# Optimization experiments

Hardware: AMD Instinct MI355X
Metric: run time of the kernel (lower is better)

Reference implementation:

```python
import jax, jax.numpy as jnp
import numpy as np

MODEL_DIM = 1024
NUM_HEADS = 16
DEPTH = MODEL_DIM // NUM_HEADS


def setup_inputs() -> dict:
    key = jax.random.key(0)
    ks = jax.random.split(key, 9)
    B, S, D = 4, 2048, MODEL_DIM
    scale = 1.0 / np.sqrt(D)
    x = jax.random.normal(ks[0], (B, S, D), dtype=jnp.float32)
    wq = jax.random.normal(ks[1], (D, D), dtype=jnp.float32) * scale
    bq = jnp.zeros((D,), dtype=jnp.float32)
    wk = jax.random.normal(ks[2], (D, D), dtype=jnp.float32) * scale
    bk = jnp.zeros((D,), dtype=jnp.float32)
    wv = jax.random.normal(ks[3], (D, D), dtype=jnp.float32) * scale
    bv = jnp.zeros((D,), dtype=jnp.float32)
    wo = jax.random.normal(ks[4], (D, D), dtype=jnp.float32) * scale
    bo = jnp.zeros((D,), dtype=jnp.float32)
    return {"x": x, "wq": wq, "bq": bq, "wk": wk, "bk": bk,
            "wv": wv, "bv": bv, "wo": wo, "bo": bo}


def reference(x, wq, bq, wk, bk, wv, bv, wo, bo):
    B, S, D = x.shape
    H, dh = NUM_HEADS, DEPTH
    # projections
    q = (x @ wq + bq).reshape(B, S, H, dh).transpose(0, 2, 1, 3)  # [B,H,S,dh]
    k = (x @ wk + bk).reshape(B, S, H, dh).transpose(0, 2, 1, 3)
    v = (x @ wv + bv).reshape(B, S, H, dh).transpose(0, 2, 1, 3)
    # scaled dot-product attention (full score matrix, as in source)
    logits = jnp.einsum('bhqd,bhkd->bhqk', q, k) / jnp.sqrt(jnp.float32(dh))
    attn = jax.nn.softmax(logits, axis=-1)
    out = jnp.einsum('bhqk,bhkd->bhqd', attn, v)  # [B,H,S,dh]
    out = out.transpose(0, 2, 1, 3).reshape(B, S, D)
    return out @ wo + bo
```

## Files before the change

kernel.cpp:

```cpp
#include <hip/hip_runtime.h>
#include <hip/hip_bf16.h>


#define S_LEN 2048
#define DMODEL 1024
#define NH 16
#define DH 64
#define BATCH 4
#define MROWS (BATCH * S_LEN)
#define NELEM_X (MROWS * DMODEL)
#define NELEM_W (DMODEL * DMODEL)
#define NELEM_B DMODEL

typedef short short8 __attribute__((ext_vector_type(8)));
typedef float floatx4 __attribute__((ext_vector_type(4)));
typedef float floatx16 __attribute__((ext_vector_type(16)));

__device__ __forceinline__ float bf2f(unsigned short u) {
    union { unsigned int i; float f; } c; c.i = ((unsigned int)u) << 16; return c.f;
}
__device__ __forceinline__ unsigned int f2bf_pk(float lo, float hi) {
    unsigned int r;
    asm("v_cvt_pk_bf16_f32 %0, %1, %2" : "=v"(r) : "v"(lo), "v"(hi));
    return r;
}
__device__ __forceinline__ void async_copy16(const void* g, void* l) {
    __builtin_amdgcn_global_load_lds(
        (const __attribute__((address_space(1))) unsigned int*)g,
        (__attribute__((address_space(3))) unsigned int*)l, 16, 0, 0);
}

__device__ __forceinline__ floatx16 mfma32_k16(short8 a, short8 b, floatx16 c) {
    return __builtin_amdgcn_mfma_f32_32x32x16_bf16(a, b, c, 0, 0, 0);
}

__global__ void sniff_kernel(const unsigned short* __restrict__ x, int* flag) {
    __shared__ int cnt;
    if (threadIdx.x == 0) cnt = 0;
    __syncthreads();
    int c = 0;
    for (int i = threadIdx.x; i < 65536; i += 256) {
        unsigned int e = (x[i] >> 7) & 0xFFu;
        if (e >= 0xC0u) c++;
    }
    atomicAdd(&cnt, c);
    __syncthreads();
    if (threadIdx.x == 0) *flag = (cnt > 64) ? 1 : 0;
}

struct ConvArgs { const void* s[5]; unsigned short* d[5]; int n8[5]; };
__global__ void convert_all(ConvArgs a, const int* __restrict__ flag) {
    const int seg = blockIdx.y;
    const int f = *flag;
    const int n8 = a.n8[seg];
    unsigned short* dst = a.d[seg];
    int i = blockIdx.x * blockDim.x + threadIdx.x;
    const int stride = gridDim.x * blockDim.x;
    if (f) {
        const float4* s4 = (const float4*)a.s[seg];
        for (; i < n8; i += stride) {
            float4 x0 = s4[2 * i], x1 = s4[2 * i + 1];
            uint4 o;
            o.x = f2bf_pk(x0.x, x0.y); o.y = f2bf_pk(x0.z, x0.w);
            o.z = f2bf_pk(x1.x, x1.y); o.w = f2bf_pk(x1.z, x1.w);
            *(uint4*)(dst + (size_t)i * 8) = o;
        }
    } else {
        const uint4* s4 = (const uint4*)a.s[seg];
        for (; i < n8; i += stride) *(uint4*)(dst + (size_t)i * 8) = s4[i];
    }
}

struct TWArgs { const void* s[4]; unsigned short* d[4]; };
__global__ void transpose_w(TWArgs a, const int* __restrict__ flag) {
    __shared__ unsigned int Lt[64 * 33];
    const int z = blockIdx.z;
    const int f = *flag;
    const int k0 = blockIdx.x * 64, n0 = blockIdx.y * 64;
    const int t = threadIdx.x;
    const int c = t & 63, rgrp = t >> 6;

    if (f) {
        const float* W = (const float*)a.s[z];
        #pragma unroll
        for (int s = 0; s < 8; s++) {
            int r0 = rgrp * 16 + 2 * s;
            float v0 = W[(size_t)(k0 + r0) * DMODEL + n0 + c];
            float v1 = W[(size_t)(k0 + r0 + 1) * DMODEL + n0 + c];
            Lt[c * 33 + rgrp * 8 + s] = f2bf_pk(v0, v1);
        }
    } else {
        const unsigned short* W = (const unsigned short*)a.s[z];
        #pragma unroll
        for (int s = 0; s < 8; s++) {
            int r0 = rgrp * 16 + 2 * s;
            unsigned int lo = W[(size_t)(k0 + r0) * DMODEL + n0 + c];
            unsigned int hi = W[(size_t)(k0 + r0 + 1) * DMODEL + n0 + c];
            Lt[c * 33 + rgrp * 8 + s] = lo | (hi << 16);
        }
    }
    __syncthreads();
    const int row = t >> 2, j = t & 3;
    unsigned int* outp = (unsigned int*)(a.d[z] + (size_t)(n0 + row) * DMODEL + k0);
    #pragma unroll
    for (int i = 0; i < 8; i++) outp[j * 8 + i] = Lt[row * 33 + j * 8 + i];
}

__global__ void transpose_v(const unsigned short* __restrict__ vws,
                            unsigned short* __restrict__ vt) {
    __shared__ unsigned int Lt[64 * 33];
    const int tok0 = blockIdx.x * 64;
    const int bh   = blockIdx.y;
    const int b    = bh >> 4;
    const int h    = bh & 15;
    const int t = threadIdx.x;
    const int c = t & 63, rgrp = t >> 6;

    const unsigned short* src = vws + (size_t)b * S_LEN * DMODEL + h * DH;
    #pragma unroll
    for (int s = 0; s < 8; s++) {
        int r0 = rgrp * 16 + 2 * s;
        unsigned int lo = src[(size_t)(tok0 + r0) * DMODEL + c];
        unsigned int hi = src[(size_t)(tok0 + r0 + 1) * DMODEL + c];
        Lt[c * 33 + rgrp * 8 + s] = lo | (hi << 16);
    }
    __syncthreads();
    const int row = t >> 2, j = t & 3;
    unsigned int* outp = (unsigned int*)(vt + (size_t)bh * DH * S_LEN
                                            + (size_t)row * S_LEN + tok0);
    const int p2[8] = {0, 1, 4, 5, 2, 3, 6, 7};
    #pragma unroll
    for (int i = 0; i < 8; i++) outp[j * 8 + i] = Lt[row * 33 + j * 8 + p2[i]];
}

__global__ __launch_bounds__(256, 2)
void gemm_bias_kernel(const unsigned short* __restrict__ X,
                      const unsigned short* __restrict__ T0, const unsigned short* __restrict__ B0, void* __restrict__ Y0,
                      const unsigned short* __restrict__ T1, const unsigned short* __restrict__ B1, void* __restrict__ Y1,
                      const unsigned short* __restrict__ T2, const unsigned short* __restrict__ B2, void* __restrict__ Y2,
                      float os0, float os1, float os2,
                      const int* __restrict__ flag, int fp32_out)
{
    const unsigned short* Wt = T0; const unsigned short* Bi = B0; void* Y = Y0;
    float os = os0;
    if (blockIdx.z == 1) { Wt = T1; Bi = B1; Y = Y1; os = os1; }
    else if (blockIdx.z == 2) { Wt = T2; Bi = B2; Y = Y2; os = os2; }
    const int f32o = fp32_out ? (*flag) : 0;

    __shared__ __align__(16) unsigned short As[128 * 32];
    __shared__ __align__(16) unsigned short Bs[128 * 32];

    const int t    = threadIdx.x;
    const int lane = t & 63;
    const int wid  = t >> 6;
    const int quad = lane >> 4;
    const int n16  = lane & 15;
    const int wm   = wid >> 1, wn = wid & 1;

    const int m0 = blockIdx.x * 128;
    const int n0 = blockIdx.y * 128;

    floatx4 acc[4][4];
    #pragma unroll
    for (int i = 0; i < 4; i++)
        #pragma unroll
        for (int j = 0; j < 4; j++) acc[i][j] = (floatx4){0.f, 0.f, 0.f, 0.f};

    const int r = t >> 2, c8 = (t & 3) * 8;

    for (int kb = 0; kb < DMODEL; kb += 32) {
        __syncthreads();
        async_copy16(X  + (size_t)(m0 + r)      * DMODEL + kb + c8, As + r * 32 + c8);
        async_copy16(X  + (size_t)(m0 + 64 + r) * DMODEL + kb + c8, As + (64 + r) * 32 + c8);
        async_copy16(Wt + (size_t)(n0 + r)      * DMODEL + kb + c8, Bs + r * 32 + c8);
        async_copy16(Wt + (size_t)(n0 + 64 + r) * DMODEL + kb + c8, Bs + (64 + r) * 32 + c8);
        __syncthreads();

        short8 af[4], bfr[4];
        #pragma unroll
        for (int mt = 0; mt < 4; mt++)
            af[mt] = *(const short8*)(As + (wm * 64 + mt * 16 + n16) * 32 + quad * 8);
        #pragma unroll
        for (int nt = 0; nt < 4; nt++)
            bfr[nt] = *(const short8*)(Bs + (wn * 64 + nt * 16 + n16) * 32 + quad * 8);
        #pragma unroll
        for (int mt = 0; mt < 4; mt++)
            #pragma unroll
            for (int nt = 0; nt < 4; nt++)
                acc[mt][nt] = __builtin_amdgcn_mfma_f32_16x16x32_bf16(af[mt], bfr[nt], acc[mt][nt], 0, 0, 0);
    }

    float bv4[4];
    #pragma unroll
    for (int nt = 0; nt < 4; nt++) bv4[nt] = bf2f(Bi[n0 + wn * 64 + nt * 16 + n16]) * os;
    #pragma unroll
    for (int mt = 0; mt < 4; mt++)
        #pragma unroll
        for (int rr = 0; rr < 4; rr++) {
            size_t row = (size_t)(m0 + wm * 64 + mt * 16 + quad * 4 + rr);
            if (f32o) {
                #pragma unroll
                for (int nt = 0; nt < 4; nt++) {
                    int col = n0 + wn * 64 + nt * 16 + n16;
                    ((float*)Y)[row * DMODEL + col] = fmaf(acc[mt][nt][rr], os, bv4[nt]);
                }
            } else {
                #pragma unroll
                for (int np = 0; np < 2; np++) {
                    float v0 = fmaf(acc[mt][2 * np    ][rr], os, bv4[2 * np]);
                    float v1 = fmaf(acc[mt][2 * np + 1][rr], os, bv4[2 * np + 1]);
                    unsigned int pk = f2bf_pk(v0, v1);
                    int col = n0 + wn * 64 + (2 * np) * 16 + n16;
                    ((unsigned short*)Y)[row * DMODEL + col]      = (unsigned short)pk;
                    ((unsigned short*)Y)[row * DMODEL + col + 16] = (unsigned short)(pk >> 16);
                }
            }
        }
}

__global__ __launch_bounds__(256, 2)
void attn_kernel(const unsigned short* Qw,
                 const unsigned short* __restrict__ Kw,
                 const unsigned short* __restrict__ VT,
                 unsigned short* Ow)
{
    __shared__ __align__(16) unsigned short Ks[64 * 64];
    __shared__ __align__(16) unsigned short Vts[64 * 64];

    const int t    = threadIdx.x;
    const int lane = t & 63;
    const int w    = t >> 6;
    const int q32  = lane & 31;
    const int hi   = lane >> 5;
    const int r7   = q32 & 7;

    const int bid  = blockIdx.x;
    const int bh   = bid & 63;
    const int qblk = bid >> 6;
    const int b    = bh >> 4;
    const int h    = bh & 15;

    const size_t baseRow = (size_t)b * S_LEN;
    const int hoff = h * DH;
    const unsigned short* VTb = VT + (size_t)bh * DH * S_LEN;

    int qrow[2];
    short8 qf[2][4];
    #pragma unroll
    for (int g = 0; g < 2; g++) {
        qrow[g] = qblk * 256 + w * 64 + g * 32 + q32;
        #pragma unroll
        for (int ds = 0; ds < 4; ds++)
            qf[g][ds] = *(const short8*)(Qw + (baseRow + qrow[g]) * DMODEL + hoff
                                            + ds * 16 + hi * 8);
    }

    const floatx16 z16 = {0.f,0.f,0.f,0.f,0.f,0.f,0.f,0.f,
                          0.f,0.f,0.f,0.f,0.f,0.f,0.f,0.f};
    const short8 ones8 = {(short)0x3F80, (short)0x3F80, (short)0x3F80, (short)0x3F80,
                          (short)0x3F80, (short)0x3F80, (short)0x3F80, (short)0x3F80};
    floatx16 acco[2][2];
    #pragma unroll
    for (int g = 0; g < 2; g++)
        #pragma unroll
        for (int dt = 0; dt < 2; dt++) acco[g][dt] = z16;
    floatx16 accl[2];
    accl[0] = z16; accl[1] = z16;

    const int srow = t >> 2;
    const int scc  = (t & 3) * 2;
    const int kswz0 = ((scc    ) ^ (srow & 7)) * 8;
    const int kswz1 = ((scc + 1) ^ (srow & 7)) * 8;
    unsigned short* KsW = Ks  + srow * 64;
    unsigned short* VsW = Vts + srow * 64;
    const unsigned short* Kp = Kw + (baseRow + srow) * DMODEL + hoff + scc * 8;
    const unsigned short* Vp = VTb + (size_t)srow * S_LEN + scc * 8;

    float4 kr0 = *(const float4*)(Kp);
    float4 kr1 = *(const float4*)(Kp + 8);
    float4 vr0 = *(const float4*)(Vp);
    float4 vr1 = *(const float4*)(Vp + 8);
    const unsigned short* KpL = Kp + (size_t)64 * DMODEL;
    const unsigned short* VpL = Vp + 64;

    for (int kb = 0; kb < S_LEN; kb += 64) {
        __syncthreads();
        *(float4*)(KsW + kswz0) = kr0;
        *(float4*)(KsW + kswz1) = kr1;
        *(float4*)(VsW + kswz0) = vr0;
        *(float4*)(VsW + kswz1) = vr1;
        if (kb + 64 < S_LEN) {
            kr0 = *(const float4*)(KpL);
            kr1 = *(const float4*)(KpL + 8);
            vr0 = *(const float4*)(VpL);
            vr1 = *(const float4*)(VpL + 8);
            KpL += (size_t)64 * DMODEL;
            VpL += 64;
        }
        __syncthreads();

        #pragma unroll
        for (int kt = 0; kt < 2; kt++) {
            const unsigned short* Kr = Ks + (kt * 32 + q32) * 64;
            floatx16 s0, s1;
            __builtin_amdgcn_s_setprio(1);
            {
                short8 kf = *(const short8*)(Kr + ((hi ^ r7) * 8));
                s0 = mfma32_k16(kf, qf[0][0], z16);
                s1 = mfma32_k16(kf, qf[1][0], z16);
            }
            #pragma unroll
            for (int ds = 1; ds < 4; ds++) {
                short8 kf = *(const short8*)(Kr + (((ds * 2 + hi) ^ r7) * 8));
                s0 = mfma32_k16(kf, qf[0][ds], s0);
                s1 = mfma32_k16(kf, qf[1][ds], s1);
            }
            __builtin_amdgcn_s_setprio(0);

            #pragma unroll
            for (int i = 0; i < 16; i++) {
                s0[i] = __builtin_exp2f(s0[i]);
                s1[i] = __builtin_exp2f(s1[i]);
            }

            __builtin_amdgcn_s_setprio(1);
            #pragma unroll
            for (int tt = 0; tt < 2; tt++) {
                union { unsigned int u[4]; short8 s8; } pb0, pb1;
                #pragma unroll
                for (int j = 0; j < 4; j++) {
                    pb0.u[j] = f2bf_pk(s0[8 * tt + 2 * j], s0[8 * tt + 2 * j + 1]);
                    pb1.u[j] = f2bf_pk(s1[8 * tt + 2 * j], s1[8 * tt + 2 * j + 1]);
                }
                const int vchunk = ((4 * kt + 2 * tt + hi) ^ r7) * 8;
                #pragma unroll
                for (int dt = 0; dt < 2; dt++) {
                    short8 vf = *(const short8*)(Vts + (dt * 32 + q32) * 64 + vchunk);
                    acco[0][dt] = mfma32_k16(vf, pb0.s8, acco[0][dt]);
                    acco[1][dt] = mfma32_k16(vf, pb1.s8, acco[1][dt]);
                }
                accl[0] = mfma32_k16(ones8, pb0.s8, accl[0]);
                accl[1] = mfma32_k16(ones8, pb1.s8, accl[1]);
            }
            __builtin_amdgcn_s_setprio(0);
        }
    }

    #pragma unroll
    for (int g = 0; g < 2; g++) {
        const float rinv = 1.f / accl[g][0];
        #pragma unroll
        for (int dt = 0; dt < 2; dt++) {
            #pragma unroll
            for (int m = 0; m < 4; m++) {
                uint2 o;
                o.x = f2bf_pk(acco[g][dt][4 * m] * rinv, acco[g][dt][4 * m + 1] * rinv);
                o.y = f2bf_pk(acco[g][dt][4 * m + 2] * rinv, acco[g][dt][4 * m + 3] * rinv);
                *(uint2*)(Ow + (baseRow + qrow[g]) * DMODEL + hoff
                             + dt * 32 + m * 8 + hi * 4) = o;
            }
        }
    }
}

extern "C" void kernel_launch(void* const* d_in, const int* in_sizes, int n_in,
                              void* d_out, int out_size, void* d_ws, size_t ws_size,
                              hipStream_t stream)
{
    unsigned short* base = (unsigned short*)d_ws;
    int* flag = (int*)d_ws;
    unsigned short* xc  = base + 8;
    unsigned short* wqt = xc  + NELEM_X;
    unsigned short* wkt = wqt + NELEM_W;
    unsigned short* wvt = wkt + NELEM_W;
    unsigned short* wot = wvt + NELEM_W;
    unsigned short* bqc = wot + NELEM_W;
    unsigned short* bkc = bqc + NELEM_B;
    unsigned short* bvc = bkc + NELEM_B;
    unsigned short* boc = bvc + NELEM_B;
    unsigned short* qws = boc + NELEM_B;
    unsigned short* kws = qws + NELEM_X;
    unsigned short* vws = kws + NELEM_X;
    unsigned short* aws = qws;
    unsigned short* vtw = xc;

    sniff_kernel<<<1, 256, 0, stream>>>((const unsigned short*)d_in[0], flag);

    ConvArgs ca;
    const void* csrc[5] = {d_in[0], d_in[2], d_in[4], d_in[6], d_in[8]};
    unsigned short* cdst[5] = {xc, bqc, bkc, bvc, boc};
    int cn8[5] = {NELEM_X / 8, NELEM_B / 8, NELEM_B / 8, NELEM_B / 8, NELEM_B / 8};
    for (int i = 0; i < 5; i++) { ca.s[i] = csrc[i]; ca.d[i] = cdst[i]; ca.n8[i] = cn8[i]; }
    convert_all<<<dim3(256, 5), 256, 0, stream>>>(ca, flag);

    TWArgs tw;
    const void* tsrc[4] = {d_in[1], d_in[3], d_in[5], d_in[7]};
    unsigned short* tdst[4] = {wqt, wkt, wvt, wot};
    for (int i = 0; i < 4; i++) { tw.s[i] = tsrc[i]; tw.d[i] = tdst[i]; }
    transpose_w<<<dim3(16, 16, 4), 256, 0, stream>>>(tw, flag);

    const float qscale = 0.125f * 1.44269504088896340736f;
    gemm_bias_kernel<<<dim3(64, 8, 3), 256, 0, stream>>>(
        xc, wqt, bqc, qws, wkt, bkc, kws, wvt, bvc, vws,
        qscale, 1.f, 1.f, flag, 0);

    transpose_v<<<dim3(32, 64), 256, 0, stream>>>(vws, vtw);

    attn_kernel<<<dim3(512), 256, 0, stream>>>(qws, kws, vtw, aws);

    gemm_bias_kernel<<<dim3(64, 8, 1), 256, 0, stream>>>(
        aws, wot, boc, d_out, wot, boc, d_out, wot, boc, d_out,
        1.f, 1.f, 1.f, flag, 1);
}
```

Baseline: 397.6 us.

## Use 512-thread attention blocks with one query group per wave and scalar row sums

The attention kernel now runs 512 threads per block, and each wave handles 32 query rows instead of 64, which halves the per-wave accumulator and Q-fragment registers so that higher occupancy is possible (launch bounds 512,4). The row-sum of exponentials is now accumulated in scalar registers and combined with a cross-half lane shuffle, replacing the extra MFMA against a ones vector. K/V tile staging is spread across twice as many threads, with one float4 each. In exchange, K/V tiles in LDS are reused by fewer query rows per wave, and more waves contend at the barriers.

```diff
diff --git a/kernel.cpp b/kernel.cpp
--- a/kernel.cpp
+++ b/kernel.cpp
@@ -218,7 +218,7 @@
         }
 }
 
-__global__ __launch_bounds__(256, 2)
+__global__ __launch_bounds__(512, 4)
 void attn_kernel(const unsigned short* Qw,
                  const unsigned short* __restrict__ Kw,
                  const unsigned short* __restrict__ VT,
@@ -244,56 +244,39 @@
     const int hoff = h * DH;
     const unsigned short* VTb = VT + (size_t)bh * DH * S_LEN;
 
-    int qrow[2];
-    short8 qf[2][4];
-    #pragma unroll
-    for (int g = 0; g < 2; g++) {
-        qrow[g] = qblk * 256 + w * 64 + g * 32 + q32;
-        #pragma unroll
-        for (int ds = 0; ds < 4; ds++)
-            qf[g][ds] = *(const short8*)(Qw + (baseRow + qrow[g]) * DMODEL + hoff
-                                            + ds * 16 + hi * 8);
-    }
+    const int qrow = qblk * 256 + w * 32 + q32;
+    short8 qf[4];
+    #pragma unroll
+    for (int ds = 0; ds < 4; ds++)
+        qf[ds] = *(const short8*)(Qw + (baseRow + qrow) * DMODEL + hoff
+                                     + ds * 16 + hi * 8);
 
     const floatx16 z16 = {0.f,0.f,0.f,0.f,0.f,0.f,0.f,0.f,
                           0.f,0.f,0.f,0.f,0.f,0.f,0.f,0.f};
-    const short8 ones8 = {(short)0x3F80, (short)0x3F80, (short)0x3F80, (short)0x3F80,
-                          (short)0x3F80, (short)0x3F80, (short)0x3F80, (short)0x3F80};
-    floatx16 acco[2][2];
-    #pragma unroll
-    for (int g = 0; g < 2; g++)
-        #pragma unroll
-        for (int dt = 0; dt < 2; dt++) acco[g][dt] = z16;
-    floatx16 accl[2];
-    accl[0] = z16; accl[1] = z16;
-
-    const int srow = t >> 2;
-    const int scc  = (t & 3) * 2;
-    const int kswz0 = ((scc    ) ^ (srow & 7)) * 8;
-    const int kswz1 = ((scc + 1) ^ (srow & 7)) * 8;
-    unsigned short* KsW = Ks  + srow * 64;
-    unsigned short* VsW = Vts + srow * 64;
+    floatx16 acco[2];
+    acco[0] = z16; acco[1] = z16;
+    float ls = 0.f;
+
+    const int srow = t >> 3;
+    const int scc  = t & 7;
+    const int kswz = (scc ^ (srow & 7)) * 8;
+    unsigned short* KsW = Ks  + srow * 64 + kswz;
+    unsigned short* VsW = Vts + srow * 64 + kswz;
     const unsigned short* Kp = Kw + (baseRow + srow) * DMODEL + hoff + scc * 8;
     const unsigned short* Vp = VTb + (size_t)srow * S_LEN + scc * 8;
 
-    float4 kr0 = *(const float4*)(Kp);
-    float4 kr1 = *(const float4*)(Kp + 8);
-    float4 vr0 = *(const float4*)(Vp);
-    float4 vr1 = *(const float4*)(Vp + 8);
+    float4 kr = *(const float4*)(Kp);
+    float4 vr = *(const float4*)(Vp);
     const unsigned short* KpL = Kp + (size_t)64 * DMODEL;
     const unsigned short* VpL = Vp + 64;
 
     for (int kb = 0; kb < S_LEN; kb += 64) {
         __syncthreads();
-        *(float4*)(KsW + kswz0) = kr0;
-        *(float4*)(KsW + kswz1) = kr1;
-        *(float4*)(VsW + kswz0) = vr0;
-        *(float4*)(VsW + kswz1) = vr1;
+        *(float4*)(KsW) = kr;
+        *(float4*)(VsW) = vr;
         if (kb + 64 < S_LEN) {
-            kr0 = *(const float4*)(KpL);
-            kr1 = *(const float4*)(KpL + 8);
-            vr0 = *(const float4*)(VpL);
-            vr1 = *(const float4*)(VpL + 8);
+            kr = *(const float4*)(KpL);
+            vr = *(const float4*)(VpL);
             KpL += (size_t)64 * DMODEL;
             VpL += 64;
         }
@@ -302,63 +285,57 @@
         #pragma unroll
         for (int kt = 0; kt < 2; kt++) {
             const unsigned short* Kr = Ks + (kt * 32 + q32) * 64;
-            floatx16 s0, s1;
+            floatx16 s;
             __builtin_amdgcn_s_setprio(1);
             {
                 short8 kf = *(const short8*)(Kr + ((hi ^ r7) * 8));
-                s0 = mfma32_k16(kf, qf[0][0], z16);
-                s1 = mfma32_k16(kf, qf[1][0], z16);
+                s = mfma32_k16(kf, qf[0], z16);
             }
             #pragma unroll
             for (int ds = 1; ds < 4; ds++) {
                 short8 kf = *(const short8*)(Kr + (((ds * 2 + hi) ^ r7) * 8));
-                s0 = mfma32_k16(kf, qf[0][ds], s0);
-                s1 = mfma32_k16(kf, qf[1][ds], s1);
+                s = mfma32_k16(kf, qf[ds], s);
             }
             __builtin_amdgcn_s_setprio(0);
 
+            float lsum = 0.f;
             #pragma unroll
             for (int i = 0; i < 16; i++) {
-                s0[i] = __builtin_exp2f(s0[i]);
-                s1[i] = __builtin_exp2f(s1[i]);
-            }
+                float p = __builtin_exp2f(s[i]);
+                s[i] = p;
+                lsum += p;
+            }
+            ls += lsum;
 
             __builtin_amdgcn_s_setprio(1);
             #pragma unroll
             for (int tt = 0; tt < 2; tt++) {
-                union { unsigned int u[4]; short8 s8; } pb0, pb1;
+                union { unsigned int u[4]; short8 s8; } pb;
                 #pragma unroll
-                for (int j = 0; j < 4; j++) {
-                    pb0.u[j] = f2bf_pk(s0[8 * tt + 2 * j], s0[8 * tt + 2 * j + 1]);
-                    pb1.u[j] = f2bf_pk(s1[8 * tt + 2 * j], s1[8 * tt + 2 * j + 1]);
-                }
+                for (int j = 0; j < 4; j++)
+                    pb.u[j] = f2bf_pk(s[8 * tt + 2 * j], s[8 * tt + 2 * j + 1]);
                 const int vchunk = ((4 * kt + 2 * tt + hi) ^ r7) * 8;
                 #pragma unroll
                 for (int dt = 0; dt < 2; dt++) {
                     short8 vf = *(const short8*)(Vts + (dt * 32 + q32) * 64 + vchunk);
-                    acco[0][dt] = mfma32_k16(vf, pb0.s8, acco[0][dt]);
-                    acco[1][dt] = mfma32_k16(vf, pb1.s8, acco[1][dt]);
+                    acco[dt] = mfma32_k16(vf, pb.s8, acco[dt]);
                 }
-                accl[0] = mfma32_k16(ones8, pb0.s8, accl[0]);
-                accl[1] = mfma32_k16(ones8, pb1.s8, accl[1]);
             }
             __builtin_amdgcn_s_setprio(0);
         }
     }
 
-    #pragma unroll
-    for (int g = 0; g < 2; g++) {
-        const float rinv = 1.f / accl[g][0];
-        #pragma unroll
-        for (int dt = 0; dt < 2; dt++) {
-            #pragma unroll
-            for (int m = 0; m < 4; m++) {
-                uint2 o;
-                o.x = f2bf_pk(acco[g][dt][4 * m] * rinv, acco[g][dt][4 * m + 1] * rinv);
-                o.y = f2bf_pk(acco[g][dt][4 * m + 2] * rinv, acco[g][dt][4 * m + 3] * rinv);
-                *(uint2*)(Ow + (baseRow + qrow[g]) * DMODEL + hoff
-                             + dt * 32 + m * 8 + hi * 4) = o;
-            }
+    float l = ls + __shfl_xor(ls, 32);
+    const float rinv = 1.f / l;
+    #pragma unroll
+    for (int dt = 0; dt < 2; dt++) {
+        #pragma unroll
+        for (int m = 0; m < 4; m++) {
+            uint2 o;
+            o.x = f2bf_pk(acco[dt][4 * m] * rinv, acco[dt][4 * m + 1] * rinv);
+            o.y = f2bf_pk(acco[dt][4 * m + 2] * rinv, acco[dt][4 * m + 3] * rinv);
+            *(uint2*)(Ow + (baseRow + qrow) * DMODEL + hoff
+                         + dt * 32 + m * 8 + hi * 4) = o;
         }
     }
 }
@@ -406,7 +383,7 @@
 
     transpose_v<<<dim3(32, 64), 256, 0, stream>>>(vws, vtw);
 
-    attn_kernel<<<dim3(512), 256, 0, stream>>>(qws, kws, vtw, aws);
+    attn_kernel<<<dim3(512), 512, 0, stream>>>(qws, kws, vtw, aws);
 
     gemm_bias_kernel<<<dim3(64, 8, 1), 256, 0, stream>>>(
         aws, wot, boc, d_out, wot, boc, d_out, wot, boc, d_out,
```

Measured after the change: 375.3 us. 5.6% less time.

## Split attention key range across wave pairs and double grid size

Applied to the files above, without the earlier changes.

Each block now handles 128 query rows instead of 256, with two waves per query group each processing half of every 64-key tile (split-K). Partial output accumulators and row sums are combined through shared memory at the end. The ones-vector MFMA used for the softmax denominator is replaced by scalar exp sums plus a lane shuffle. The grid is doubled to 1024 blocks and launch bounds raised to 3 blocks per SIMD to improve occupancy, at the cost of an extra reduction epilogue and more K/V tile loads per query row.

```diff
diff --git a/kernel.cpp b/kernel.cpp
--- a/kernel.cpp
+++ b/kernel.cpp
@@ -218,7 +218,7 @@
         }
 }
 
-__global__ __launch_bounds__(256, 2)
+__global__ __launch_bounds__(256, 3)
 void attn_kernel(const unsigned short* Qw,
                  const unsigned short* __restrict__ Kw,
                  const unsigned short* __restrict__ VT,
@@ -226,10 +226,13 @@
 {
     __shared__ __align__(16) unsigned short Ks[64 * 64];
     __shared__ __align__(16) unsigned short Vts[64 * 64];
+    __shared__ float Lsh[2 * 64];
 
     const int t    = threadIdx.x;
     const int lane = t & 63;
     const int w    = t >> 6;
+    const int qgrp = w >> 1;
+    const int kth  = w & 1;
     const int q32  = lane & 31;
     const int hi   = lane >> 5;
     const int r7   = q32 & 7;
@@ -248,7 +251,7 @@
     short8 qf[2][4];
     #pragma unroll
     for (int g = 0; g < 2; g++) {
-        qrow[g] = qblk * 256 + w * 64 + g * 32 + q32;
+        qrow[g] = qblk * 128 + qgrp * 64 + g * 32 + q32;
         #pragma unroll
         for (int ds = 0; ds < 4; ds++)
             qf[g][ds] = *(const short8*)(Qw + (baseRow + qrow[g]) * DMODEL + hoff
@@ -257,15 +260,12 @@
 
     const floatx16 z16 = {0.f,0.f,0.f,0.f,0.f,0.f,0.f,0.f,
                           0.f,0.f,0.f,0.f,0.f,0.f,0.f,0.f};
-    const short8 ones8 = {(short)0x3F80, (short)0x3F80, (short)0x3F80, (short)0x3F80,
-                          (short)0x3F80, (short)0x3F80, (short)0x3F80, (short)0x3F80};
     floatx16 acco[2][2];
     #pragma unroll
     for (int g = 0; g < 2; g++)
         #pragma unroll
         for (int dt = 0; dt < 2; dt++) acco[g][dt] = z16;
-    floatx16 accl[2];
-    accl[0] = z16; accl[1] = z16;
+    float ls[2] = {0.f, 0.f};
 
     const int srow = t >> 2;
     const int scc  = (t & 3) * 2;
@@ -299,67 +299,119 @@
         }
         __syncthreads();
 
-        #pragma unroll
-        for (int kt = 0; kt < 2; kt++) {
-            const unsigned short* Kr = Ks + (kt * 32 + q32) * 64;
-            floatx16 s0, s1;
-            __builtin_amdgcn_s_setprio(1);
-            {
-                short8 kf = *(const short8*)(Kr + ((hi ^ r7) * 8));
-                s0 = mfma32_k16(kf, qf[0][0], z16);
-                s1 = mfma32_k16(kf, qf[1][0], z16);
-            }
-            #pragma unroll
-            for (int ds = 1; ds < 4; ds++) {
-                short8 kf = *(const short8*)(Kr + (((ds * 2 + hi) ^ r7) * 8));
-                s0 = mfma32_k16(kf, qf[0][ds], s0);
-                s1 = mfma32_k16(kf, qf[1][ds], s1);
-            }
-            __builtin_amdgcn_s_setprio(0);
-
+        const unsigned short* Kr = Ks + (kth * 32 + q32) * 64;
+        floatx16 s0, s1;
+        __builtin_amdgcn_s_setprio(1);
+        {
+            short8 kf = *(const short8*)(Kr + ((hi ^ r7) * 8));
+            s0 = mfma32_k16(kf, qf[0][0], z16);
+            s1 = mfma32_k16(kf, qf[1][0], z16);
+        }
+        #pragma unroll
+        for (int ds = 1; ds < 4; ds++) {
+            short8 kf = *(const short8*)(Kr + (((ds * 2 + hi) ^ r7) * 8));
+            s0 = mfma32_k16(kf, qf[0][ds], s0);
+            s1 = mfma32_k16(kf, qf[1][ds], s1);
+        }
+        __builtin_amdgcn_s_setprio(0);
+
+        float l0 = 0.f, l1 = 0.f;
+        #pragma unroll
+        for (int i = 0; i < 16; i++) {
+            float p0 = __builtin_exp2f(s0[i]);
+            float p1 = __builtin_exp2f(s1[i]);
+            s0[i] = p0; s1[i] = p1;
+            l0 += p0; l1 += p1;
+        }
+        ls[0] += l0; ls[1] += l1;
+
+        __builtin_amdgcn_s_setprio(1);
+        #pragma unroll
+        for (int tt = 0; tt < 2; tt++) {
+            union { unsigned int u[4]; short8 s8; } pb0, pb1;
+            #pragma unroll
+            for (int j = 0; j < 4; j++) {
+                pb0.u[j] = f2bf_pk(s0[8 * tt + 2 * j], s0[8 * tt + 2 * j + 1]);
+                pb1.u[j] = f2bf_pk(s1[8 * tt + 2 * j], s1[8 * tt + 2 * j + 1]);
+            }
+            const int vchunk = ((4 * kth + 2 * tt + hi) ^ r7) * 8;
+            #pragma unroll
+            for (int dt = 0; dt < 2; dt++) {
+                short8 vf = *(const short8*)(Vts + (dt * 32 + q32) * 64 + vchunk);
+                acco[0][dt] = mfma32_k16(vf, pb0.s8, acco[0][dt]);
+                acco[1][dt] = mfma32_k16(vf, pb1.s8, acco[1][dt]);
+            }
+        }
+        __builtin_amdgcn_s_setprio(0);
+    }
+
+    float l32[2];
+    #pragma unroll
+    for (int g = 0; g < 2; g++) l32[g] = ls[g] + __shfl_xor(ls[g], 32);
+
+    float* M = (qgrp == 0) ? (float*)Ks : (float*)Vts;
+    float rinv[2] = {0.f, 0.f};
+
+    __syncthreads();
+    if (kth) {
+        #pragma unroll
+        for (int g = 0; g < 2; g++)
             #pragma unroll
             for (int i = 0; i < 16; i++) {
-                s0[i] = __builtin_exp2f(s0[i]);
-                s1[i] = __builtin_exp2f(s1[i]);
-            }
-
-            __builtin_amdgcn_s_setprio(1);
-            #pragma unroll
-            for (int tt = 0; tt < 2; tt++) {
-                union { unsigned int u[4]; short8 s8; } pb0, pb1;
-                #pragma unroll
-                for (int j = 0; j < 4; j++) {
-                    pb0.u[j] = f2bf_pk(s0[8 * tt + 2 * j], s0[8 * tt + 2 * j + 1]);
-                    pb1.u[j] = f2bf_pk(s1[8 * tt + 2 * j], s1[8 * tt + 2 * j + 1]);
-                }
-                const int vchunk = ((4 * kt + 2 * tt + hi) ^ r7) * 8;
-                #pragma unroll
-                for (int dt = 0; dt < 2; dt++) {
-                    short8 vf = *(const short8*)(Vts + (dt * 32 + q32) * 64 + vchunk);
-                    acco[0][dt] = mfma32_k16(vf, pb0.s8, acco[0][dt]);
-                    acco[1][dt] = mfma32_k16(vf, pb1.s8, acco[1][dt]);
-                }
-                accl[0] = mfma32_k16(ones8, pb0.s8, accl[0]);
-                accl[1] = mfma32_k16(ones8, pb1.s8, accl[1]);
-            }
-            __builtin_amdgcn_s_setprio(0);
-        }
-    }
-
-    #pragma unroll
-    for (int g = 0; g < 2; g++) {
-        const float rinv = 1.f / accl[g][0];
-        #pragma unroll
-        for (int dt = 0; dt < 2; dt++) {
+                const int d = 4 * hi + (i & 3) + 8 * (i >> 2);
+                M[d * 64 + g * 32 + q32] = acco[g][0][i];
+            }
+        if (!hi) {
+            Lsh[qgrp * 64 + q32]      = l32[0];
+            Lsh[qgrp * 64 + 32 + q32] = l32[1];
+        }
+    }
+    __syncthreads();
+    if (!kth) {
+        #pragma unroll
+        for (int g = 0; g < 2; g++)
+            rinv[g] = 1.f / (l32[g] + Lsh[qgrp * 64 + g * 32 + q32]);
+        #pragma unroll
+        for (int g = 0; g < 2; g++)
             #pragma unroll
             for (int m = 0; m < 4; m++) {
+                float v0 = acco[g][0][4 * m    ] + M[(4 * hi     + 8 * m) * 64 + g * 32 + q32];
+                float v1 = acco[g][0][4 * m + 1] + M[(4 * hi + 1 + 8 * m) * 64 + g * 32 + q32];
+                float v2 = acco[g][0][4 * m + 2] + M[(4 * hi + 2 + 8 * m) * 64 + g * 32 + q32];
+                float v3 = acco[g][0][4 * m + 3] + M[(4 * hi + 3 + 8 * m) * 64 + g * 32 + q32];
                 uint2 o;
-                o.x = f2bf_pk(acco[g][dt][4 * m] * rinv, acco[g][dt][4 * m + 1] * rinv);
-                o.y = f2bf_pk(acco[g][dt][4 * m + 2] * rinv, acco[g][dt][4 * m + 3] * rinv);
+                o.x = f2bf_pk(v0 * rinv[g], v1 * rinv[g]);
+                o.y = f2bf_pk(v2 * rinv[g], v3 * rinv[g]);
                 *(uint2*)(Ow + (baseRow + qrow[g]) * DMODEL + hoff
-                             + dt * 32 + m * 8 + hi * 4) = o;
-            }
-        }
+                             + m * 8 + hi * 4) = o;
+            }
+    }
+    __syncthreads();
+    if (kth) {
+        #pragma unroll
+        for (int g = 0; g < 2; g++)
+            #pragma unroll
+            for (int i = 0; i < 16; i++) {
+                const int d = 4 * hi + (i & 3) + 8 * (i >> 2);
+                M[d * 64 + g * 32 + q32] = acco[g][1][i];
+            }
+    }
+    __syncthreads();
+    if (!kth) {
+        #pragma unroll
+        for (int g = 0; g < 2; g++)
+            #pragma unroll
+            for (int m = 0; m < 4; m++) {
+                float v0 = acco[g][1][4 * m    ] + M[(4 * hi     + 8 * m) * 64 + g * 32 + q32];
+                float v1 = acco[g][1][4 * m + 1] + M[(4 * hi + 1 + 8 * m) * 64 + g * 32 + q32];
+                float v2 = acco[g][1][4 * m + 2] + M[(4 * hi + 2 + 8 * m) * 64 + g * 32 + q32];
+                float v3 = acco[g][1][4 * m + 3] + M[(4 * hi + 3 + 8 * m) * 64 + g * 32 + q32];
+                uint2 o;
+                o.x = f2bf_pk(v0 * rinv[g], v1 * rinv[g]);
+                o.y = f2bf_pk(v2 * rinv[g], v3 * rinv[g]);
+                *(uint2*)(Ow + (baseRow + qrow[g]) * DMODEL + hoff
+                             + 32 + m * 8 + hi * 4) = o;
+            }
     }
 }
 
@@ -406,7 +458,7 @@
 
     transpose_v<<<dim3(32, 64), 256, 0, stream>>>(vws, vtw);
 
-    attn_kernel<<<dim3(512), 256, 0, stream>>>(qws, kws, vtw, aws);
+    attn_kernel<<<dim3(1024), 256, 0, stream>>>(qws, kws, vtw, aws);
 
     gemm_bias_kernel<<<dim3(64, 8, 1), 256, 0, stream>>>(
         aws, wot, boc, d_out, wot, boc, d_out, wot, boc, d_out,
```

After: 395.5 us. Within noise of the previous version (-0.5%).
